# Optimization experiments

Hardware: AMD Instinct MI355X
Metric: run time of the kernel (lower is better)

Reference implementation:

```python
import jax, jax.numpy as jnp
import numpy as np

POS_NUM = 60
TWO_PI = 2.0 * np.pi


def setup_inputs() -> dict:
    key = jax.random.key(0)
    k1, k2 = jax.random.split(key)
    B = 262144
    # [r1, r3, r4, r5, thc]; positive link lengths / angle in a realistic range
    pred_tensor = jax.random.uniform(k1, (B, 5), minval=0.1, maxval=2.0, dtype=jnp.float32)
    target_tensor = jax.random.normal(k2, (B, 2 * POS_NUM), dtype=jnp.float32)
    return {"pred_tensor": pred_tensor, "target_tensor": target_tensor}


def _compute_pos(pred, th2_min, th2_max, n):
    """Vectorized version of PosLoss.compute_pos.
    pred: [B,9] = [r1,r2,r3,r4,th1,r5,alpha,x0,y0]; th2_min/th2_max: [B].
    Returns interleaved coupler positions [B, 2n] = [x0,y0,x1,y1,...]."""
    dt = pred.dtype
    step = (th2_max - th2_min) / (n - 1)                     # [B]
    th2 = th2_min[:, None] + step[:, None] * jnp.arange(n, dtype=dt)  # [B,n]
    r1, r2, r3, r4 = pred[:, 0:1], pred[:, 1:2], pred[:, 2:3], pred[:, 3:4]
    th1, r5, al = pred[:, 4:5], pred[:, 5:6], pred[:, 6:7]
    x0, y0 = pred[:, 7:8], pred[:, 8:9]
    k1 = r1**2 + r2**2 + r3**2 - r4**2 - 2.0 * r1 * r2 * jnp.cos(th2 - th1)
    k2 = 2.0 * r1 * r3 * jnp.cos(th1) - 2.0 * r2 * r3 * jnp.cos(th2)
    k3 = 2.0 * r1 * r3 * jnp.sin(th1) - 2.0 * r2 * r3 * jnp.sin(th2)
    a = k1 + k2
    b = -2.0 * k3
    c = k1 - k2
    disc = b * b - 4.0 * a * c
    bad = disc < 0                                            # == isnan(sqrt(disc))
    D = jnp.sqrt(jnp.where(bad, 0.0, disc))
    th3 = 2.0 * jnp.arctan((-b + D) / (2.0 * a))
    p1x = jnp.where(bad, 0.0, r2 * jnp.cos(th2) + r5 * jnp.cos(al + th3) + x0)
    p1y = jnp.where(bad, 0.0, r2 * jnp.sin(th2) + r5 * jnp.sin(al + th3) + y0)
    return jnp.stack([p1x, p1y], axis=-1).reshape(pred.shape[0], 2 * n)


def reference(pred_tensor, target_tensor):
    n = POS_NUM
    dt = pred_tensor.dtype
    B = pred_tensor.shape[0]
    zeros = jnp.zeros((B,), dt)
    ones = jnp.ones((B,), dt)
    # pred9 = [r1, r2=1, r3, r4, th1=0, r5, alpha=thc, x0=0, y0=0]
    pred9 = jnp.stack([pred_tensor[:, 0], ones, pred_tensor[:, 1], pred_tensor[:, 2],
                       zeros, pred_tensor[:, 3], pred_tensor[:, 4], zeros, zeros], axis=1)
    L = pred9[:, :4]
    valid = 2.0 * jnp.max(L, axis=1) < jnp.sum(L, axis=1)
    c1 = (L[:, 0] + L[:, 1] - (L[:, 2] + L[:, 3])) > 0
    c2 = (jnp.abs(L[:, 0] - L[:, 1]) - jnp.abs(L[:, 2] - L[:, 3])) >= 0
    up = valid & c1 & c2
    low = valid & (~c1) & (~c2)
    bo = valid & c1 & (~c2)
    no = valid & (~c1) & c2
    denom = 2.0 * L[:, 0] * L[:, 1]
    arg_sum = (L[:, 0] ** 2 + L[:, 1] ** 2 - (L[:, 2] + L[:, 3]) ** 2) / denom
    arg_diff = (L[:, 0] ** 2 + L[:, 1] ** 2 - (L[:, 2] - L[:, 3]) ** 2) / denom
    acos_sum = jnp.arccos(jnp.where(up | bo, arg_sum, 0.0))
    acos_diff = jnp.arccos(jnp.where(low | bo, arg_diff, 0.0))
    th2_min = jnp.where(up, -acos_sum, jnp.where(low | bo, acos_diff, 0.0))
    th2_max = jnp.where(up | bo, acos_sum, jnp.where(low, TWO_PI - acos_diff, TWO_PI))
    # Sanitize rows that never contribute (invalid) so no NaN/Inf leaks in.
    safe_row = jnp.asarray([2.0, 1.0, 2.0, 2.0, 0.0, 1.0, 0.0, 0.0, 0.0], dt)
    pred_eff = jnp.where(valid[:, None], pred9, safe_row)
    th2_min = jnp.where(valid, th2_min, 0.0)
    th2_max = jnp.where(valid, th2_max, TWO_PI)
    pos = _compute_pos(pred_eff, th2_min, th2_max, n)         # [B, 2n]
    sq = (pos - target_tensor) ** 2

    def msum(m, x):
        return jnp.sum(jnp.where(m[:, None], x, 0.0))

    invalid_loss = msum(~valid, target_tensor ** 2)           # pos == 0 for invalid rows
    up_loss = msum(up, sq)
    low_loss = msum(low, sq)
    bo_loss = msum(bo, sq)
    no_loss = msum(no, sq)
    Nf = jnp.asarray(B, dt)
    return (invalid_loss / Nf, up_loss / Nf, low_loss / Nf, bo_loss / Nf, no_loss / Nf)
```

## Files before the change

### kernel.cpp

```cpp
#include <hip/hip_runtime.h>
#include <math.h>

#define CHUNK 32
#define NPOS 60
#define TWO_PI_F 6.283185307179586f
#define INV_TWO_PI_F 0.15915494309189535f
#define PI_F 3.14159265358979f

__device__ __forceinline__ float bcastf(float v, int l) {
    return __builtin_bit_cast(float, __builtin_amdgcn_readlane(__builtin_bit_cast(int, v), l));
}

__device__ __forceinline__ float acos_poly(float x) {
    const float ax = fabsf(x);
    const float s = __builtin_amdgcn_sqrtf(fmaxf(0.0f, 1.0f - ax));
    float p = fmaf(ax, -0.0187293f, 0.0742610f);
    p = fmaf(ax, p, -0.2121144f);
    p = fmaf(ax, p, 1.5707288f);
    const float r = s * p;
    return (x < 0.0f) ? (PI_F - r) : r;
}

__device__ __forceinline__ void hw_sincos_rev(float rev, float* s, float* c) {
    const float f = __builtin_amdgcn_fractf(rev);
    *s = __builtin_amdgcn_sinf(f);
    *c = __builtin_amdgcn_cosf(f);
}

__device__ __forceinline__ void row_acc(
    int rr, float txj, float tyj, float flane, bool inpos,
    float th2min_rev, float stp_rev, float ca5, float sa5,
    float P, float Q, float R, float S, float Bb, int cat,
    float& a0, float& a1, float& a2, float& a3, float& a4)
{
    const int catr    = __builtin_amdgcn_readlane(cat, rr);
    const float rev0  = bcastf(th2min_rev, rr);
    const float stp_r = bcastf(stp_rev, rr);
    const float ca5_r = bcastf(ca5, rr);
    const float sa5_r = bcastf(sa5, rr);
    const float P_r   = bcastf(P, rr);
    const float Q_r   = bcastf(Q, rr);
    const float R_r   = bcastf(R, rr);
    const float S_r   = bcastf(S, rr);
    const float Bb_r  = bcastf(Bb, rr);

    const float rev = fmaf(stp_r, flane, rev0);
    float sth, cth;
    hw_sincos_rev(rev, &sth, &cth);
    const float a  = fmaf(-Q_r, cth, P_r);
    const float cc = fmaf(-S_r, cth, R_r);
    const float b  = Bb_r * sth;
    const float disc = fmaf(b, b, -4.0f * (a * cc));
    const bool bad = disc < 0.0f;
    const float D = __builtin_amdgcn_sqrtf(fmaxf(disc, 0.0f));
    const float w = D - b;
    const float s = a + a;
    const float s2 = s * s, w2 = w * w;
    const float rden = __builtin_amdgcn_rcpf(s2 + w2);
    const float c3 = (s2 - w2) * rden;
    const float sw = s * w;
    const float s3 = (sw + sw) * rden;
    float px = fmaf(ca5_r, c3, fmaf(-sa5_r, s3, cth));
    float py = fmaf(sa5_r, c3, fmaf(ca5_r, s3, sth));
    px = bad ? 0.0f : px;
    py = bad ? 0.0f : py;
    const float dx = px - txj, dy = py - tyj;
    float ch = fmaf(dx, dx, dy * dy);
    ch = inpos ? ch : 0.0f;
    float c0 = fmaf(txj, txj, tyj * tyj);
    c0 = inpos ? c0 : 0.0f;
    a0 += (catr == 0) ? c0 : 0.0f;
    a1 += (catr == 1) ? ch : 0.0f;
    a2 += (catr == 2) ? ch : 0.0f;
    a3 += (catr == 3) ? ch : 0.0f;
    a4 += (catr == 4) ? ch : 0.0f;
}

__device__ __forceinline__ float2 ldt(const float* __restrict__ target,
                                      int base, int rr, int lpos) {
    return *reinterpret_cast<const float2*>(
        target + (size_t)(base + rr) * (size_t)(2 * NPOS) + 2 * lpos);
}

#define LOADB(Pfx, r0)                                                                 \
    do {                                                                               \
        float2 _v;                                                                     \
        _v = ldt(target, base, (r0) + 0, lpos); Pfx##x0 = _v.x; Pfx##y0 = _v.y;        \
        _v = ldt(target, base, (r0) + 1, lpos); Pfx##x1 = _v.x; Pfx##y1 = _v.y;        \
        _v = ldt(target, base, (r0) + 2, lpos); Pfx##x2 = _v.x; Pfx##y2 = _v.y;        \
        _v = ldt(target, base, (r0) + 3, lpos); Pfx##x3 = _v.x; Pfx##y3 = _v.y;        \
        _v = ldt(target, base, (r0) + 4, lpos); Pfx##x4 = _v.x; Pfx##y4 = _v.y;        \
        _v = ldt(target, base, (r0) + 5, lpos); Pfx##x5 = _v.x; Pfx##y5 = _v.y;        \
        _v = ldt(target, base, (r0) + 6, lpos); Pfx##x6 = _v.x; Pfx##y6 = _v.y;        \
        _v = ldt(target, base, (r0) + 7, lpos); Pfx##x7 = _v.x; Pfx##y7 = _v.y;        \
    } while (0)

#define ROWA(Pfx, rr, sx, sy)                                                          \
    row_acc((rr), Pfx##sx, Pfx##sy, flane, inpos, th2min_rev, stp_rev, ca5, sa5,       \
            Pc, Qc, Rc, Sc, Bb, cat, a0, a1, a2, a3, a4)

#define COMPUTEB(Pfx, r0)                                                              \
    do {                                                                               \
        ROWA(Pfx, (r0) + 0, x0, y0);                                                   \
        ROWA(Pfx, (r0) + 1, x1, y1);                                                   \
        ROWA(Pfx, (r0) + 2, x2, y2);                                                   \
        ROWA(Pfx, (r0) + 3, x3, y3);                                                   \
        ROWA(Pfx, (r0) + 4, x4, y4);                                                   \
        ROWA(Pfx, (r0) + 5, x5, y5);                                                   \
        ROWA(Pfx, (r0) + 6, x6, y6);                                                   \
        ROWA(Pfx, (r0) + 7, x7, y7);                                                   \
    } while (0)

__global__ __launch_bounds__(256, 6) void posloss_main(
    const float* __restrict__ pred, const float* __restrict__ target,
    float* __restrict__ partials, int B, int nchunks)
{
    const int tid  = threadIdx.x;
    const int lane = tid & 63;
    const int wv   = tid >> 6;
    const int wid  = (blockIdx.x * blockDim.x + tid) >> 6;
    const bool inpos = lane < NPOS;
    const int lpos = inpos ? lane : (NPOS - 1);
    const float flane = (float)lane;

    float a0 = 0.f, a1 = 0.f, a2 = 0.f, a3 = 0.f, a4 = 0.f;

    if (wid < nchunks) {
        const int base = wid * CHUNK;
        const int rmax = (B - base) < CHUNK ? (B - base) : CHUNK;

        const int prow = base + (lane & 31);
        float r1 = 2.f, r3 = 2.f, r4 = 2.f, r5 = 1.f, al = 0.f;
        if (prow < B) {
            const float* pp = pred + (size_t)prow * 5;
            r1 = pp[0]; r3 = pp[1]; r4 = pp[2]; r5 = pp[3]; al = pp[4];
        }

        const float sumL = ((r1 + 1.0f) + r3) + r4;
        const float maxL = fmaxf(fmaxf(r1, 1.0f), fmaxf(r3, r4));
        const bool valid = (2.0f * maxL) < sumL;
        const bool c1 = ((r1 + 1.0f) - (r3 + r4)) > 0.0f;
        const bool c2 = (fabsf(r1 - 1.0f) - fabsf(r3 - r4)) >= 0.0f;
        const bool up = valid && c1 && c2;
        const bool lo = valid && (!c1) && (!c2);
        const bool bo = valid && c1 && (!c2);
        const float rdenom = __builtin_amdgcn_rcpf(2.0f * r1);
        const float s34 = r3 + r4, d34 = r3 - r4;
        const float r1sq1 = fmaf(r1, r1, 1.0f);
        float argS = (r1sq1 - s34 * s34) * rdenom;
        float argD = (r1sq1 - d34 * d34) * rdenom;
        argS = (up || bo) ? argS : 0.0f;
        argD = (lo || bo) ? argD : 0.0f;
        argS = fminf(1.0f, fmaxf(-1.0f, argS));
        argD = fminf(1.0f, fmaxf(-1.0f, argD));
        const float acS = acos_poly(argS);
        const float acD = acos_poly(argD);
        float th2min = up ? (-acS) : ((lo || bo) ? acD : 0.0f);
        float th2max = (up || bo) ? acS : (lo ? (TWO_PI_F - acD) : TWO_PI_F);
        if (!valid) { th2min = 0.0f; th2max = TWO_PI_F; }
        const float stp_rev    = (th2max - th2min) * (INV_TWO_PI_F / 59.0f);
        const float th2min_rev = th2min * INV_TWO_PI_F;
        const int cat = (!valid) ? 0 : (up ? 1 : (lo ? 2 : (bo ? 3 : 4)));
        float sal, cal;
        hw_sincos_rev(al * INV_TWO_PI_F, &sal, &cal);
        const float ca5 = r5 * cal, sa5 = r5 * sal;
        const float K1c = fmaf(r3, r3, r1sq1) - r4 * r4;
        const float K1m = 2.0f * r1;
        const float A2  = (2.0f * r1) * r3;
        const float B2  = 2.0f * r3;
        const float Pc = K1c + A2;
        const float Qc = K1m + B2;
        const float Rc = K1c - A2;
        const float Sc = K1m - B2;
        const float Bb = 2.0f * B2;

        if (rmax == CHUNK) {
            float Ax0,Ay0,Ax1,Ay1,Ax2,Ay2,Ax3,Ay3,Ax4,Ay4,Ax5,Ay5,Ax6,Ay6,Ax7,Ay7;
            float Bx0,By0,Bx1,By1,Bx2,By2,Bx3,By3,Bx4,By4,Bx5,By5,Bx6,By6,Bx7,By7;
            LOADB(A, 0);
            LOADB(B, 8);
            COMPUTEB(A, 0);
            LOADB(A, 16);
            COMPUTEB(B, 8);
            LOADB(B, 24);
            COMPUTEB(A, 16);
            COMPUTEB(B, 24);
        } else {
            for (int rr = 0; rr < rmax; ++rr) {
                const float2 tv = ldt(target, base, rr, lpos);
                row_acc(rr, tv.x, tv.y, flane, inpos, th2min_rev, stp_rev, ca5, sa5,
                        Pc, Qc, Rc, Sc, Bb, cat, a0, a1, a2, a3, a4);
            }
        }
    }

    for (int off = 32; off; off >>= 1) {
        a0 += __shfl_xor(a0, off);
        a1 += __shfl_xor(a1, off);
        a2 += __shfl_xor(a2, off);
        a3 += __shfl_xor(a3, off);
        a4 += __shfl_xor(a4, off);
    }
    __shared__ float red[4][5];
    if (lane == 0) {
        red[wv][0] = a0; red[wv][1] = a1; red[wv][2] = a2; red[wv][3] = a3; red[wv][4] = a4;
    }
    __syncthreads();
    if (tid < 5) {
        const float s = ((red[0][tid] + red[1][tid]) + red[2][tid]) + red[3][tid];
        partials[(size_t)tid * gridDim.x + blockIdx.x] = s;
    }
}

__global__ void posloss_reduce(const float* __restrict__ partials, float* __restrict__ out,
                               int nblocks, int B)
{
    const int w = threadIdx.x >> 6, lane = threadIdx.x & 63;
    if (w >= 5) return;
    double s0 = 0.0, s1 = 0.0, s2 = 0.0, s3 = 0.0;
    const float* p = partials + (size_t)w * nblocks;
    for (int k = lane; k + 192 < nblocks; k += 256) {
        s0 += (double)p[k];
        s1 += (double)p[k + 64];
        s2 += (double)p[k + 128];
        s3 += (double)p[k + 192];
    }
    double s = (s0 + s1) + (s2 + s3);
    for (int off = 32; off; off >>= 1) s += __shfl_down(s, off);
    if (lane == 0) out[w] = (float)(s / (double)B);
}

extern "C" void kernel_launch(void* const* d_in, const int* in_sizes, int n_in,
                              void* d_out, int out_size, void* d_ws, size_t ws_size,
                              hipStream_t stream) {
    (void)n_in; (void)out_size; (void)ws_size;
    const float* pred   = (const float*)d_in[0];
    const float* target = (const float*)d_in[1];
    float* out = (float*)d_out;
    float* partials = (float*)d_ws;
    const int B = in_sizes[0] / 5;
    const int nchunks = (B + CHUNK - 1) / CHUNK;
    const int nblocks = 2048;
    posloss_main<<<nblocks, 256, 0, stream>>>(pred, target, partials, B, nchunks);
    posloss_reduce<<<1, 320, 0, stream>>>(partials, out, nblocks, B);
}
```

Measured before the change: 39.52 us.

## Skip trig for invalid rows and fold final reduction into atomics

Rows in category 0 (invalid) now take an early return that only adds the squared target norm, skipping the sincos, sqrt and reciprocal work. The scalar readlane makes this branch wave-uniform. The accumulator selects become if/else chains. The separate reduce kernel is replaced by per-block atomicAdd of pre-scaled sums into a zeroed output, and the grid is sized to exactly cover all chunks instead of a fixed 2048 blocks. This removes a kernel launch but adds a memset, makes float summation order nondeterministic, and changes how work is spread across blocks.

```diff
diff --git a/kernel.cpp b/kernel.cpp
--- a/kernel.cpp
+++ b/kernel.cpp
@@ -33,7 +33,12 @@
     float P, float Q, float R, float S, float Bb, int cat,
     float& a0, float& a1, float& a2, float& a3, float& a4)
 {
-    const int catr    = __builtin_amdgcn_readlane(cat, rr);
+    const int catr = __builtin_amdgcn_readlane(cat, rr);
+    if (catr == 0) {
+        float c0 = fmaf(txj, txj, tyj * tyj);
+        a0 += inpos ? c0 : 0.0f;
+        return;
+    }
     const float rev0  = bcastf(th2min_rev, rr);
     const float stp_r = bcastf(stp_rev, rr);
     const float ca5_r = bcastf(ca5, rr);
@@ -67,13 +72,10 @@
     const float dx = px - txj, dy = py - tyj;
     float ch = fmaf(dx, dx, dy * dy);
     ch = inpos ? ch : 0.0f;
-    float c0 = fmaf(txj, txj, tyj * tyj);
-    c0 = inpos ? c0 : 0.0f;
-    a0 += (catr == 0) ? c0 : 0.0f;
-    a1 += (catr == 1) ? ch : 0.0f;
-    a2 += (catr == 2) ? ch : 0.0f;
-    a3 += (catr == 3) ? ch : 0.0f;
-    a4 += (catr == 4) ? ch : 0.0f;
+    if      (catr == 1) a1 += ch;
+    else if (catr == 2) a2 += ch;
+    else if (catr == 3) a3 += ch;
+    else                a4 += ch;
 }
 
 __device__ __forceinline__ float2 ldt(const float* __restrict__ target,
@@ -113,7 +115,7 @@
 
 __global__ __launch_bounds__(256, 6) void posloss_main(
     const float* __restrict__ pred, const float* __restrict__ target,
-    float* __restrict__ partials, int B, int nchunks)
+    float* __restrict__ out, int B, int nchunks)
 {
     const int tid  = threadIdx.x;
     const int lane = tid & 63;
@@ -208,39 +210,21 @@
     __syncthreads();
     if (tid < 5) {
         const float s = ((red[0][tid] + red[1][tid]) + red[2][tid]) + red[3][tid];
-        partials[(size_t)tid * gridDim.x + blockIdx.x] = s;
-    }
-}
-
-__global__ void posloss_reduce(const float* __restrict__ partials, float* __restrict__ out,
-                               int nblocks, int B)
-{
-    const int w = threadIdx.x >> 6, lane = threadIdx.x & 63;
-    if (w >= 5) return;
-    double s0 = 0.0, s1 = 0.0, s2 = 0.0, s3 = 0.0;
-    const float* p = partials + (size_t)w * nblocks;
-    for (int k = lane; k + 192 < nblocks; k += 256) {
-        s0 += (double)p[k];
-        s1 += (double)p[k + 64];
-        s2 += (double)p[k + 128];
-        s3 += (double)p[k + 192];
-    }
-    double s = (s0 + s1) + (s2 + s3);
-    for (int off = 32; off; off >>= 1) s += __shfl_down(s, off);
-    if (lane == 0) out[w] = (float)(s / (double)B);
+        const float invB = 1.0f / (float)B;
+        atomicAdd(&out[tid], s * invB);
+    }
 }
 
 extern "C" void kernel_launch(void* const* d_in, const int* in_sizes, int n_in,
                               void* d_out, int out_size, void* d_ws, size_t ws_size,
                               hipStream_t stream) {
-    (void)n_in; (void)out_size; (void)ws_size;
+    (void)n_in; (void)out_size; (void)d_ws; (void)ws_size;
     const float* pred   = (const float*)d_in[0];
     const float* target = (const float*)d_in[1];
     float* out = (float*)d_out;
-    float* partials = (float*)d_ws;
     const int B = in_sizes[0] / 5;
     const int nchunks = (B + CHUNK - 1) / CHUNK;
-    const int nblocks = 2048;
-    posloss_main<<<nblocks, 256, 0, stream>>>(pred, target, partials, B, nchunks);
-    posloss_reduce<<<1, 320, 0, stream>>>(partials, out, nblocks, B);
-}
+    const int nblocks = (nchunks + 3) / 4;
+    hipMemsetAsync(out, 0, 5 * sizeof(float), stream);
+    posloss_main<<<nblocks, 256, 0, stream>>>(pred, target, out, B, nchunks);
+}
```

Result: slower. 61.43 us (+55.4%).

## Issue all target loads up front and overlap with per-row setup math

Applied to the files above, without the earlier changes.

The full-chunk path now issues all four 8-row batches of target loads before computing, instead of double-buffering two batches, and moves the per-row parameter setup (acos, sincos, coefficients) after the loads so it hides their latency. The setup math is duplicated into the tail path. Launch bounds drop from 6 to 4 waves per SIMD to leave room for the extra 32 live registers, trading occupancy for more memory-level parallelism per wave.

```diff
diff --git a/kernel.cpp b/kernel.cpp
--- a/kernel.cpp
+++ b/kernel.cpp
@@ -111,7 +111,7 @@
         ROWA(Pfx, (r0) + 7, x7, y7);                                                   \
     } while (0)
 
-__global__ __launch_bounds__(256, 6) void posloss_main(
+__global__ __launch_bounds__(256, 4) void posloss_main(
     const float* __restrict__ pred, const float* __restrict__ target,
     float* __restrict__ partials, int B, int nchunks)
 {
@@ -136,56 +136,97 @@
             r1 = pp[0]; r3 = pp[1]; r4 = pp[2]; r5 = pp[3]; al = pp[4];
         }
 
-        const float sumL = ((r1 + 1.0f) + r3) + r4;
-        const float maxL = fmaxf(fmaxf(r1, 1.0f), fmaxf(r3, r4));
-        const bool valid = (2.0f * maxL) < sumL;
-        const bool c1 = ((r1 + 1.0f) - (r3 + r4)) > 0.0f;
-        const bool c2 = (fabsf(r1 - 1.0f) - fabsf(r3 - r4)) >= 0.0f;
-        const bool up = valid && c1 && c2;
-        const bool lo = valid && (!c1) && (!c2);
-        const bool bo = valid && c1 && (!c2);
-        const float rdenom = __builtin_amdgcn_rcpf(2.0f * r1);
-        const float s34 = r3 + r4, d34 = r3 - r4;
-        const float r1sq1 = fmaf(r1, r1, 1.0f);
-        float argS = (r1sq1 - s34 * s34) * rdenom;
-        float argD = (r1sq1 - d34 * d34) * rdenom;
-        argS = (up || bo) ? argS : 0.0f;
-        argD = (lo || bo) ? argD : 0.0f;
-        argS = fminf(1.0f, fmaxf(-1.0f, argS));
-        argD = fminf(1.0f, fmaxf(-1.0f, argD));
-        const float acS = acos_poly(argS);
-        const float acD = acos_poly(argD);
-        float th2min = up ? (-acS) : ((lo || bo) ? acD : 0.0f);
-        float th2max = (up || bo) ? acS : (lo ? (TWO_PI_F - acD) : TWO_PI_F);
-        if (!valid) { th2min = 0.0f; th2max = TWO_PI_F; }
-        const float stp_rev    = (th2max - th2min) * (INV_TWO_PI_F / 59.0f);
-        const float th2min_rev = th2min * INV_TWO_PI_F;
-        const int cat = (!valid) ? 0 : (up ? 1 : (lo ? 2 : (bo ? 3 : 4)));
-        float sal, cal;
-        hw_sincos_rev(al * INV_TWO_PI_F, &sal, &cal);
-        const float ca5 = r5 * cal, sa5 = r5 * sal;
-        const float K1c = fmaf(r3, r3, r1sq1) - r4 * r4;
-        const float K1m = 2.0f * r1;
-        const float A2  = (2.0f * r1) * r3;
-        const float B2  = 2.0f * r3;
-        const float Pc = K1c + A2;
-        const float Qc = K1m + B2;
-        const float Rc = K1c - A2;
-        const float Sc = K1m - B2;
-        const float Bb = 2.0f * B2;
-
         if (rmax == CHUNK) {
             float Ax0,Ay0,Ax1,Ay1,Ax2,Ay2,Ax3,Ay3,Ax4,Ay4,Ax5,Ay5,Ax6,Ay6,Ax7,Ay7;
             float Bx0,By0,Bx1,By1,Bx2,By2,Bx3,By3,Bx4,By4,Bx5,By5,Bx6,By6,Bx7,By7;
+            float Cx0,Cy0,Cx1,Cy1,Cx2,Cy2,Cx3,Cy3,Cx4,Cy4,Cx5,Cy5,Cx6,Cy6,Cx7,Cy7;
+            float Dx0,Dy0,Dx1,Dy1,Dx2,Dy2,Dx3,Dy3,Dx4,Dy4,Dx5,Dy5,Dx6,Dy6,Dx7,Dy7;
             LOADB(A, 0);
             LOADB(B, 8);
+            LOADB(C, 16);
+            LOADB(D, 24);
+
+            const float sumL = ((r1 + 1.0f) + r3) + r4;
+            const float maxL = fmaxf(fmaxf(r1, 1.0f), fmaxf(r3, r4));
+            const bool valid = (2.0f * maxL) < sumL;
+            const bool c1 = ((r1 + 1.0f) - (r3 + r4)) > 0.0f;
+            const bool c2 = (fabsf(r1 - 1.0f) - fabsf(r3 - r4)) >= 0.0f;
+            const bool up = valid && c1 && c2;
+            const bool lo = valid && (!c1) && (!c2);
+            const bool bo = valid && c1 && (!c2);
+            const float rdenom = __builtin_amdgcn_rcpf(2.0f * r1);
+            const float s34 = r3 + r4, d34 = r3 - r4;
+            const float r1sq1 = fmaf(r1, r1, 1.0f);
+            float argS = (r1sq1 - s34 * s34) * rdenom;
+            float argD = (r1sq1 - d34 * d34) * rdenom;
+            argS = (up || bo) ? argS : 0.0f;
+            argD = (lo || bo) ? argD : 0.0f;
+            argS = fminf(1.0f, fmaxf(-1.0f, argS));
+            argD = fminf(1.0f, fmaxf(-1.0f, argD));
+            const float acS = acos_poly(argS);
+            const float acD = acos_poly(argD);
+            float th2min = up ? (-acS) : ((lo || bo) ? acD : 0.0f);
+            float th2max = (up || bo) ? acS : (lo ? (TWO_PI_F - acD) : TWO_PI_F);
+            if (!valid) { th2min = 0.0f; th2max = TWO_PI_F; }
+            const float stp_rev    = (th2max - th2min) * (INV_TWO_PI_F / 59.0f);
+            const float th2min_rev = th2min * INV_TWO_PI_F;
+            const int cat = (!valid) ? 0 : (up ? 1 : (lo ? 2 : (bo ? 3 : 4)));
+            float sal, cal;
+            hw_sincos_rev(al * INV_TWO_PI_F, &sal, &cal);
+            const float ca5 = r5 * cal, sa5 = r5 * sal;
+            const float K1c = fmaf(r3, r3, r1sq1) - r4 * r4;
+            const float K1m = 2.0f * r1;
+            const float A2  = (2.0f * r1) * r3;
+            const float B2  = 2.0f * r3;
+            const float Pc = K1c + A2;
+            const float Qc = K1m + B2;
+            const float Rc = K1c - A2;
+            const float Sc = K1m - B2;
+            const float Bb = 2.0f * B2;
+
             COMPUTEB(A, 0);
-            LOADB(A, 16);
             COMPUTEB(B, 8);
-            LOADB(B, 24);
-            COMPUTEB(A, 16);
-            COMPUTEB(B, 24);
+            COMPUTEB(C, 16);
+            COMPUTEB(D, 24);
         } else {
+            const float sumL = ((r1 + 1.0f) + r3) + r4;
+            const float maxL = fmaxf(fmaxf(r1, 1.0f), fmaxf(r3, r4));
+            const bool valid = (2.0f * maxL) < sumL;
+            const bool c1 = ((r1 + 1.0f) - (r3 + r4)) > 0.0f;
+            const bool c2 = (fabsf(r1 - 1.0f) - fabsf(r3 - r4)) >= 0.0f;
+            const bool up = valid && c1 && c2;
+            const bool lo = valid && (!c1) && (!c2);
+            const bool bo = valid && c1 && (!c2);
+            const float rdenom = __builtin_amdgcn_rcpf(2.0f * r1);
+            const float s34 = r3 + r4, d34 = r3 - r4;
+            const float r1sq1 = fmaf(r1, r1, 1.0f);
+            float argS = (r1sq1 - s34 * s34) * rdenom;
+            float argD = (r1sq1 - d34 * d34) * rdenom;
+            argS = (up || bo) ? argS : 0.0f;
+            argD = (lo || bo) ? argD : 0.0f;
+            argS = fminf(1.0f, fmaxf(-1.0f, argS));
+            argD = fminf(1.0f, fmaxf(-1.0f, argD));
+            const float acS = acos_poly(argS);
+            const float acD = acos_poly(argD);
+            float th2min = up ? (-acS) : ((lo || bo) ? acD : 0.0f);
+            float th2max = (up || bo) ? acS : (lo ? (TWO_PI_F - acD) : TWO_PI_F);
+            if (!valid) { th2min = 0.0f; th2max = TWO_PI_F; }
+            const float stp_rev    = (th2max - th2min) * (INV_TWO_PI_F / 59.0f);
+            const float th2min_rev = th2min * INV_TWO_PI_F;
+            const int cat = (!valid) ? 0 : (up ? 1 : (lo ? 2 : (bo ? 3 : 4)));
+            float sal, cal;
+            hw_sincos_rev(al * INV_TWO_PI_F, &sal, &cal);
+            const float ca5 = r5 * cal, sa5 = r5 * sal;
+            const float K1c = fmaf(r3, r3, r1sq1) - r4 * r4;
+            const float K1m = 2.0f * r1;
+            const float A2  = (2.0f * r1) * r3;
+            const float B2  = 2.0f * r3;
+            const float Pc = K1c + A2;
+            const float Qc = K1m + B2;
+            const float Rc = K1c - A2;
+            const float Sc = K1m - B2;
+            const float Bb = 2.0f * B2;
+
             for (int rr = 0; rr < rmax; ++rr) {
                 const float2 tv = ldt(target, base, rr, lpos);
                 row_acc(rr, tv.x, tv.y, flane, inpos, th2min_rev, stp_rev, ca5, sa5,
```

Result: no change. 39.49 us (-0.1%).

## Process two chunks per wave with software-pipelined loads across chunks

Applied to the files above, without the earlier changes.

Each wave now handles two 32-row chunks, striding by the total wave count, and the grid is halved to 1024 blocks. The target loads and pred loads for the second chunk are issued while the first chunk's rows are still being computed, so memory latency at the chunk boundary is hidden. The per-row setup is factored into macros. The cost is higher register pressure from the extra live pred values, and fewer waves in flight overall.

```diff
diff --git a/kernel.cpp b/kernel.cpp
--- a/kernel.cpp
+++ b/kernel.cpp
@@ -82,17 +82,17 @@
         target + (size_t)(base + rr) * (size_t)(2 * NPOS) + 2 * lpos);
 }
 
-#define LOADB(Pfx, r0)                                                                 \
+#define LOADB(Pfx, bb, r0)                                                             \
     do {                                                                               \
         float2 _v;                                                                     \
-        _v = ldt(target, base, (r0) + 0, lpos); Pfx##x0 = _v.x; Pfx##y0 = _v.y;        \
-        _v = ldt(target, base, (r0) + 1, lpos); Pfx##x1 = _v.x; Pfx##y1 = _v.y;        \
-        _v = ldt(target, base, (r0) + 2, lpos); Pfx##x2 = _v.x; Pfx##y2 = _v.y;        \
-        _v = ldt(target, base, (r0) + 3, lpos); Pfx##x3 = _v.x; Pfx##y3 = _v.y;        \
-        _v = ldt(target, base, (r0) + 4, lpos); Pfx##x4 = _v.x; Pfx##y4 = _v.y;        \
-        _v = ldt(target, base, (r0) + 5, lpos); Pfx##x5 = _v.x; Pfx##y5 = _v.y;        \
-        _v = ldt(target, base, (r0) + 6, lpos); Pfx##x6 = _v.x; Pfx##y6 = _v.y;        \
-        _v = ldt(target, base, (r0) + 7, lpos); Pfx##x7 = _v.x; Pfx##y7 = _v.y;        \
+        _v = ldt(target, (bb), (r0) + 0, lpos); Pfx##x0 = _v.x; Pfx##y0 = _v.y;        \
+        _v = ldt(target, (bb), (r0) + 1, lpos); Pfx##x1 = _v.x; Pfx##y1 = _v.y;        \
+        _v = ldt(target, (bb), (r0) + 2, lpos); Pfx##x2 = _v.x; Pfx##y2 = _v.y;        \
+        _v = ldt(target, (bb), (r0) + 3, lpos); Pfx##x3 = _v.x; Pfx##y3 = _v.y;        \
+        _v = ldt(target, (bb), (r0) + 4, lpos); Pfx##x4 = _v.x; Pfx##y4 = _v.y;        \
+        _v = ldt(target, (bb), (r0) + 5, lpos); Pfx##x5 = _v.x; Pfx##y5 = _v.y;        \
+        _v = ldt(target, (bb), (r0) + 6, lpos); Pfx##x6 = _v.x; Pfx##y6 = _v.y;        \
+        _v = ldt(target, (bb), (r0) + 7, lpos); Pfx##x7 = _v.x; Pfx##y7 = _v.y;        \
     } while (0)
 
 #define ROWA(Pfx, rr, sx, sy)                                                          \
@@ -111,6 +111,53 @@
         ROWA(Pfx, (r0) + 7, x7, y7);                                                   \
     } while (0)
 
+#define PROLOGUE(r1_, r3_, r4_, r5_, al_)                                              \
+    do {                                                                               \
+        const float sumL = ((r1_ + 1.0f) + r3_) + r4_;                                 \
+        const float maxL = fmaxf(fmaxf(r1_, 1.0f), fmaxf(r3_, r4_));                   \
+        const bool valid = (2.0f * maxL) < sumL;                                       \
+        const bool c1 = ((r1_ + 1.0f) - (r3_ + r4_)) > 0.0f;                           \
+        const bool c2 = (fabsf(r1_ - 1.0f) - fabsf(r3_ - r4_)) >= 0.0f;                \
+        const bool up = valid && c1 && c2;                                             \
+        const bool lo = valid && (!c1) && (!c2);                                       \
+        const bool bo = valid && c1 && (!c2);                                          \
+        const float rdenom = __builtin_amdgcn_rcpf(2.0f * r1_);                        \
+        const float s34 = r3_ + r4_, d34 = r3_ - r4_;                                  \
+        const float r1sq1 = fmaf(r1_, r1_, 1.0f);                                      \
+        float argS = (r1sq1 - s34 * s34) * rdenom;                                     \
+        float argD = (r1sq1 - d34 * d34) * rdenom;                                     \
+        argS = (up || bo) ? argS : 0.0f;                                               \
+        argD = (lo || bo) ? argD : 0.0f;                                               \
+        argS = fminf(1.0f, fmaxf(-1.0f, argS));                                        \
+        argD = fminf(1.0f, fmaxf(-1.0f, argD));                                        \
+        const float acS = acos_poly(argS);                                             \
+        const float acD = acos_poly(argD);                                             \
+        float th2min = up ? (-acS) : ((lo || bo) ? acD : 0.0f);                        \
+        float th2max = (up || bo) ? acS : (lo ? (TWO_PI_F - acD) : TWO_PI_F);          \
+        if (!valid) { th2min = 0.0f; th2max = TWO_PI_F; }                              \
+        stp_rev    = (th2max - th2min) * (INV_TWO_PI_F / 59.0f);                       \
+        th2min_rev = th2min * INV_TWO_PI_F;                                            \
+        cat = (!valid) ? 0 : (up ? 1 : (lo ? 2 : (bo ? 3 : 4)));                       \
+        float sal, cal;                                                                \
+        hw_sincos_rev(al_ * INV_TWO_PI_F, &sal, &cal);                                 \
+        ca5 = r5_ * cal; sa5 = r5_ * sal;                                              \
+        const float K1c = fmaf(r3_, r3_, r1sq1) - r4_ * r4_;                           \
+        const float K1m = 2.0f * r1_;                                                  \
+        const float A2  = (2.0f * r1_) * r3_;                                          \
+        const float B2  = 2.0f * r3_;                                                  \
+        Pc = K1c + A2; Qc = K1m + B2; Rc = K1c - A2; Sc = K1m - B2; Bb = 2.0f * B2;    \
+    } while (0)
+
+#define LOADPRED(r1_, r3_, r4_, r5_, al_, bb)                                          \
+    do {                                                                               \
+        const int prow_ = (bb) + (lane & 31);                                          \
+        r1_ = 2.f; r3_ = 2.f; r4_ = 2.f; r5_ = 1.f; al_ = 0.f;                         \
+        if (prow_ < B) {                                                               \
+            const float* pp_ = pred + (size_t)prow_ * 5;                               \
+            r1_ = pp_[0]; r3_ = pp_[1]; r4_ = pp_[2]; r5_ = pp_[3]; al_ = pp_[4];      \
+        }                                                                              \
+    } while (0)
+
 __global__ __launch_bounds__(256, 6) void posloss_main(
     const float* __restrict__ pred, const float* __restrict__ target,
     float* __restrict__ partials, int B, int nchunks)
@@ -119,73 +166,54 @@
     const int lane = tid & 63;
     const int wv   = tid >> 6;
     const int wid  = (blockIdx.x * blockDim.x + tid) >> 6;
+    const int nw   = (gridDim.x * blockDim.x) >> 6;
     const bool inpos = lane < NPOS;
     const int lpos = inpos ? lane : (NPOS - 1);
     const float flane = (float)lane;
 
     float a0 = 0.f, a1 = 0.f, a2 = 0.f, a3 = 0.f, a4 = 0.f;
 
-    if (wid < nchunks) {
-        const int base = wid * CHUNK;
-        const int rmax = (B - base) < CHUNK ? (B - base) : CHUNK;
-
-        const int prow = base + (lane & 31);
-        float r1 = 2.f, r3 = 2.f, r4 = 2.f, r5 = 1.f, al = 0.f;
-        if (prow < B) {
-            const float* pp = pred + (size_t)prow * 5;
-            r1 = pp[0]; r3 = pp[1]; r4 = pp[2]; r5 = pp[3]; al = pp[4];
-        }
-
-        const float sumL = ((r1 + 1.0f) + r3) + r4;
-        const float maxL = fmaxf(fmaxf(r1, 1.0f), fmaxf(r3, r4));
-        const bool valid = (2.0f * maxL) < sumL;
-        const bool c1 = ((r1 + 1.0f) - (r3 + r4)) > 0.0f;
-        const bool c2 = (fabsf(r1 - 1.0f) - fabsf(r3 - r4)) >= 0.0f;
-        const bool up = valid && c1 && c2;
-        const bool lo = valid && (!c1) && (!c2);
-        const bool bo = valid && c1 && (!c2);
-        const float rdenom = __builtin_amdgcn_rcpf(2.0f * r1);
-        const float s34 = r3 + r4, d34 = r3 - r4;
-        const float r1sq1 = fmaf(r1, r1, 1.0f);
-        float argS = (r1sq1 - s34 * s34) * rdenom;
-        float argD = (r1sq1 - d34 * d34) * rdenom;
-        argS = (up || bo) ? argS : 0.0f;
-        argD = (lo || bo) ? argD : 0.0f;
-        argS = fminf(1.0f, fmaxf(-1.0f, argS));
-        argD = fminf(1.0f, fmaxf(-1.0f, argD));
-        const float acS = acos_poly(argS);
-        const float acD = acos_poly(argD);
-        float th2min = up ? (-acS) : ((lo || bo) ? acD : 0.0f);
-        float th2max = (up || bo) ? acS : (lo ? (TWO_PI_F - acD) : TWO_PI_F);
-        if (!valid) { th2min = 0.0f; th2max = TWO_PI_F; }
-        const float stp_rev    = (th2max - th2min) * (INV_TWO_PI_F / 59.0f);
-        const float th2min_rev = th2min * INV_TWO_PI_F;
-        const int cat = (!valid) ? 0 : (up ? 1 : (lo ? 2 : (bo ? 3 : 4)));
-        float sal, cal;
-        hw_sincos_rev(al * INV_TWO_PI_F, &sal, &cal);
-        const float ca5 = r5 * cal, sa5 = r5 * sal;
-        const float K1c = fmaf(r3, r3, r1sq1) - r4 * r4;
-        const float K1m = 2.0f * r1;
-        const float A2  = (2.0f * r1) * r3;
-        const float B2  = 2.0f * r3;
-        const float Pc = K1c + A2;
-        const float Qc = K1m + B2;
-        const float Rc = K1c - A2;
-        const float Sc = K1m - B2;
-        const float Bb = 2.0f * B2;
-
-        if (rmax == CHUNK) {
-            float Ax0,Ay0,Ax1,Ay1,Ax2,Ay2,Ax3,Ay3,Ax4,Ay4,Ax5,Ay5,Ax6,Ay6,Ax7,Ay7;
-            float Bx0,By0,Bx1,By1,Bx2,By2,Bx3,By3,Bx4,By4,Bx5,By5,Bx6,By6,Bx7,By7;
-            LOADB(A, 0);
-            LOADB(B, 8);
-            COMPUTEB(A, 0);
-            LOADB(A, 16);
-            COMPUTEB(B, 8);
-            LOADB(B, 24);
-            COMPUTEB(A, 16);
-            COMPUTEB(B, 24);
-        } else {
+    float th2min_rev, stp_rev, ca5, sa5, Pc, Qc, Rc, Sc, Bb;
+    int cat;
+
+    const int c0 = wid;
+    const int c1 = wid + nw;
+    const int base0 = c0 * CHUNK;
+    const int base1 = c1 * CHUNK;
+    const bool full0 = (c0 < nchunks) && (B - base0 >= CHUNK);
+    const bool full1 = (c1 < nchunks) && (B - base1 >= CHUNK);
+
+    if (full0 && full1) {
+        float pr1, pr3, pr4, pr5, pal;
+        float qr1, qr3, qr4, qr5, qal;
+        float Ax0,Ay0,Ax1,Ay1,Ax2,Ay2,Ax3,Ay3,Ax4,Ay4,Ax5,Ay5,Ax6,Ay6,Ax7,Ay7;
+        float Bx0,By0,Bx1,By1,Bx2,By2,Bx3,By3,Bx4,By4,Bx5,By5,Bx6,By6,Bx7,By7;
+
+        LOADPRED(pr1, pr3, pr4, pr5, pal, base0);
+        LOADB(A, base0, 0);
+        LOADB(B, base0, 8);
+        PROLOGUE(pr1, pr3, pr4, pr5, pal);
+
+        COMPUTEB(A, 0);  LOADB(A, base0, 16);
+        COMPUTEB(B, 8);  LOADB(B, base0, 24);
+                         LOADPRED(qr1, qr3, qr4, qr5, qal, base1);
+        COMPUTEB(A, 16); LOADB(A, base1, 0);
+        COMPUTEB(B, 24); LOADB(B, base1, 8);
+
+        PROLOGUE(qr1, qr3, qr4, qr5, qal);
+        COMPUTEB(A, 0);  LOADB(A, base1, 16);
+        COMPUTEB(B, 8);  LOADB(B, base1, 24);
+        COMPUTEB(A, 16);
+        COMPUTEB(B, 24);
+    } else {
+        for (int k = 0; k < 2; ++k) {
+            const int c = (k == 0) ? c0 : c1;
+            if (c >= nchunks) continue;
+            const int base = c * CHUNK;
+            const int rmax = (B - base) < CHUNK ? (B - base) : CHUNK;
+            float pr1, pr3, pr4, pr5, pal;
+            LOADPRED(pr1, pr3, pr4, pr5, pal, base);
+            PROLOGUE(pr1, pr3, pr4, pr5, pal);
             for (int rr = 0; rr < rmax; ++rr) {
                 const float2 tv = ldt(target, base, rr, lpos);
                 row_acc(rr, tv.x, tv.y, flane, inpos, th2min_rev, stp_rev, ca5, sa5,
@@ -240,7 +268,7 @@
     float* partials = (float*)d_ws;
     const int B = in_sizes[0] / 5;
     const int nchunks = (B + CHUNK - 1) / CHUNK;
-    const int nblocks = 2048;
+    const int nblocks = 1024;
     posloss_main<<<nblocks, 256, 0, stream>>>(pred, target, partials, B, nchunks);
     posloss_reduce<<<1, 320, 0, stream>>>(partials, out, nblocks, B);
 }
```

Measured after the change: 55.35 us. 40.1% more time.
